# Kernel optimization log

Measured on AMD Instinct MI355X. Metric: run time of the kernel, lower is better.

Reference implementation:

```python
import jax, jax.numpy as jnp
import numpy as np

N = 12288
IN_C = 64
OUT_C = 64
NEG_INF = -1.0e9

def setup_inputs() -> dict:
    key = jax.random.key(0)
    k1, k2, k3, k4 = jax.random.split(key, 4)
    x = jax.random.normal(k1, (N, IN_C), dtype=jnp.float32)
    edge_index = jax.random.randint(k2, (N, N), 0, 2, dtype=jnp.int32)
    # xavier-ish scaling for params
    weight_w = jax.random.normal(k3, (IN_C, OUT_C), dtype=jnp.float32) * (1.0 / np.sqrt(IN_C))
    weight_a = jax.random.normal(k4, (2 * OUT_C, 1), dtype=jnp.float32) * (1.0 / np.sqrt(OUT_C))
    bias = jnp.zeros((OUT_C,), dtype=jnp.float32)
    return {"x": x, "edge_index": edge_index, "weight_w": weight_w,
            "weight_a": weight_a, "bias": bias}

def reference(x, edge_index, weight_w, weight_a, bias):
    wh = x @ weight_w                              # [N, out]
    a_src = weight_a[:OUT_C, 0]                    # [out]
    a_dst = weight_a[OUT_C:, 0]                    # [out]
    # rank-1 additive score: e[i,j] = <wh_i, a_src> + <wh_j, a_dst>
    e = (wh @ a_src)[:, None] + (wh @ a_dst)[None, :]   # [N, N]
    e = jax.nn.leaky_relu(e, negative_slope=0.01)        # torch LeakyReLU default
    scores = jnp.where(edge_index > 0, e, NEG_INF)
    attention = jax.nn.softmax(scores, axis=1)           # row-wise
    out = attention @ wh                                  # [N, out]
    return out + bias
```

## Files before the change

### kernel.cpp

```cpp
#include <hip/hip_runtime.h>
#include <hip/hip_bf16.h>
#include <cstddef>
#include <cstdint>

#define Nn 12288
#define MSTRIDE 264
#define DSTOFF (2 * 16 * MSTRIDE)
#define LOG2E 1.44269504088896340736f

typedef __bf16 bf16x8 __attribute__((ext_vector_type(8)));
typedef float  f32x4  __attribute__((ext_vector_type(4)));
typedef int    i32x4  __attribute__((ext_vector_type(4)));

__device__ __forceinline__ void gload_lds16_nt(const void* g, void* l) {
    __builtin_amdgcn_global_load_lds(
        (const __attribute__((address_space(1))) void*)g,
        (__attribute__((address_space(3))) void*)l, 16, 0, 2 );
}
__device__ __forceinline__ void gload_lds4(const void* g, void* l) {
    __builtin_amdgcn_global_load_lds(
        (const __attribute__((address_space(1))) void*)g,
        (__attribute__((address_space(3))) void*)l, 4, 0, 0);
}

__global__ __launch_bounds__(256) void prep_kernel(
    const float* __restrict__ x, const float* __restrict__ W,
    const float* __restrict__ wa, __bf16* __restrict__ whB,
    float* __restrict__ src, float* __restrict__ dst)
{
    __shared__ float  Wl[64 * 64];
    __shared__ float  Xl[64 * 64];
    __shared__ __bf16 whl[64 * 72];
    int t = threadIdx.x;
    int R0 = blockIdx.x * 64;
    for (int i = t; i < 4096; i += 256) {
        Wl[i] = W[i];
        Xl[i] = x[(size_t)R0 * 64 + i];
    }
    __syncthreads();
    int c   = t & 63;
    int r16 = (t >> 6) * 16;
    float vals[16];
    #pragma unroll
    for (int k = 0; k < 16; ++k) vals[k] = 0.f;
    #pragma unroll 16
    for (int kk = 0; kk < 64; ++kk) {
        float wv = Wl[kk * 64 + c];
        #pragma unroll
        for (int k = 0; k < 16; ++k)
            vals[k] = fmaf(Xl[(r16 + k) * 64 + kk], wv, vals[k]);
    }
    #pragma unroll
    for (int k = 0; k < 16; ++k) whl[c * 72 + r16 + k] = (__bf16)vals[k];
    __syncthreads();
    if (t < 64) {
        float s = 0.f, d = 0.f;
        #pragma unroll 16
        for (int cc = 0; cc < 64; ++cc) {
            float v = (float)whl[cc * 72 + t];
            s = fmaf(v, wa[cc], s);
            d = fmaf(v, wa[64 + cc], d);
        }
        src[R0 + t] = s * LOG2E;
        dst[R0 + t] = d * LOG2E;
    }
    #pragma unroll
    for (int gg = 0; gg < 2; ++gg) {
        int gidx   = t * 2 + gg;
        int jc_loc = gidx >> 8;
        int q      = (gidx >> 6) & 3;
        int lane   = gidx & 63;
        int crow   = (lane & 15) + 16 * q;
        int jrow   = jc_loc * 32 + (lane >> 4) * 8;
        bf16x8 v = *(const bf16x8*)&whl[crow * 72 + jrow];
        int jc = blockIdx.x * 2 + jc_loc;
        *(bf16x8*)&whB[((size_t)(jc * 4 + q) * 64 + lane) * 8] = v;
    }
}

__global__ __launch_bounds__(256) void attn_kernel(
    const int* __restrict__ mask, const __bf16* __restrict__ whB,
    const float* __restrict__ src, const float* __restrict__ dstv,
    const float* __restrict__ bias, float* __restrict__ out)
{
    __shared__ int lm[DSTOFF + 2 * 256];

    int t    = threadIdx.x;
    int lane = t & 63;
    int wid  = t >> 6;
    int g    = blockIdx.x;
    int row  = lane & 15;
    int kg   = lane >> 4;
    int jl   = kg * 8;

    float srow = src[g * 16 + row];
    asm volatile("" :: "v"(srow));

    bf16x8 vones;
    #pragma unroll
    for (int e = 0; e < 8; ++e) vones[e] = (__bf16)1.0f;

    i32x4 bset[2][8];
    f32x4 acc0 = {0.f, 0.f, 0.f, 0.f}, acc1 = acc0, acc2 = acc0, acc3 = acc0;
    f32x4 accZ = acc0;

#define STAGE(B, TT)                                                          \
    do {                                                                      \
        _Pragma("unroll")                                                     \
        for (int rr = 0; rr < 4; ++rr) {                                      \
            int rs = wid * 4 + rr;                                            \
            gload_lds16_nt(mask + (size_t)(g * 16 + rs) * Nn + (TT) * 256 +   \
                               lane * 4,                                      \
                           &lm[(B) * 4224 + rs * MSTRIDE]);                   \
        }                                                                     \
        gload_lds4(dstv + (TT) * 256 + wid * 64 + lane,                       \
                   &lm[DSTOFF + (B) * 256 + wid * 64]);                       \
    } while (0)

#define BLOAD(P, TT)                                                          \
    do {                                                                      \
        const char* _b0 = (const char*)whB +                                  \
                          ((size_t)((TT) * 8 + wid * 2)) * 4096 +             \
                          (size_t)lane * 16;                                  \
        const char* _b1 = _b0 + 4096;                                         \
        asm volatile("global_load_dwordx4 %0, %1, off"                        \
                     : "=v"(bset[P][0]) : "v"(_b0));                          \
        asm volatile("global_load_dwordx4 %0, %1, off offset:1024"            \
                     : "=v"(bset[P][1]) : "v"(_b0));                          \
        asm volatile("global_load_dwordx4 %0, %1, off offset:2048"            \
                     : "=v"(bset[P][2]) : "v"(_b0));                          \
        asm volatile("global_load_dwordx4 %0, %1, off offset:3072"            \
                     : "=v"(bset[P][3]) : "v"(_b0));                          \
        asm volatile("global_load_dwordx4 %0, %1, off"                        \
                     : "=v"(bset[P][4]) : "v"(_b1));                          \
        asm volatile("global_load_dwordx4 %0, %1, off offset:1024"            \
                     : "=v"(bset[P][5]) : "v"(_b1));                          \
        asm volatile("global_load_dwordx4 %0, %1, off offset:2048"            \
                     : "=v"(bset[P][6]) : "v"(_b1));                          \
        asm volatile("global_load_dwordx4 %0, %1, off offset:3072"            \
                     : "=v"(bset[P][7]) : "v"(_b1));                          \
    } while (0)

#define COMPUTE(TT, B, P)                                                     \
    do {                                                                      \
        const int*   mb = &lm[(B) * 4224 + row * MSTRIDE + wid * 64];         \
        const float* db = (const float*)&lm[DSTOFF + (B) * 256 + wid * 64];   \
        _Pragma("unroll")                                                     \
        for (int cc = 0; cc < 2; ++cc) {                                      \
            i32x4 m0 = *(const i32x4*)(mb + cc * 32 + jl);                    \
            i32x4 m1 = *(const i32x4*)(mb + cc * 32 + jl + 4);                \
            f32x4 d0 = *(const f32x4*)(db + cc * 32 + jl);                    \
            f32x4 d1 = *(const f32x4*)(db + cc * 32 + jl + 4);                \
            bf16x8 pa;                                                        \
            _Pragma("unroll")                                                 \
            for (int e = 0; e < 4; ++e) {                                     \
                float t0 = srow + d0[e];                                      \
                float f0 = fmaxf(t0, 0.01f * t0);                             \
                float w0 = __builtin_amdgcn_exp2f(f0);                        \
                w0 = (m0[e] > 0) ? w0 : 0.f;                                  \
                pa[e] = (__bf16)w0;                                           \
                float t1 = srow + d1[e];                                      \
                float f1 = fmaxf(t1, 0.01f * t1);                             \
                float w1 = __builtin_amdgcn_exp2f(f1);                        \
                w1 = (m1[e] > 0) ? w1 : 0.f;                                  \
                pa[4 + e] = (__bf16)w1;                                       \
            }                                                                 \
            acc0 = __builtin_amdgcn_mfma_f32_16x16x32_bf16(                   \
                pa, __builtin_bit_cast(bf16x8, bset[P][cc * 4 + 0]), acc0, 0, 0, 0); \
            acc1 = __builtin_amdgcn_mfma_f32_16x16x32_bf16(                   \
                pa, __builtin_bit_cast(bf16x8, bset[P][cc * 4 + 1]), acc1, 0, 0, 0); \
            acc2 = __builtin_amdgcn_mfma_f32_16x16x32_bf16(                   \
                pa, __builtin_bit_cast(bf16x8, bset[P][cc * 4 + 2]), acc2, 0, 0, 0); \
            acc3 = __builtin_amdgcn_mfma_f32_16x16x32_bf16(                   \
                pa, __builtin_bit_cast(bf16x8, bset[P][cc * 4 + 3]), acc3, 0, 0, 0); \
            accZ = __builtin_amdgcn_mfma_f32_16x16x32_bf16(                   \
                pa, vones, accZ, 0, 0, 0);                                    \
        }                                                                     \
    } while (0)

#define BODY_FULL(P)                                                          \
    do {                                                                      \
        STAGE((P) ^ 1, tt + 1);                                               \
        BLOAD((P) ^ 1, tt + 1);                                               \
        asm volatile("s_waitcnt vmcnt(13)" ::: "memory");                     \
        __builtin_amdgcn_sched_barrier(0);                                    \
        __builtin_amdgcn_s_barrier();                                         \
        __builtin_amdgcn_sched_barrier(0);                                    \
        COMPUTE(tt, P, P);                                                    \
        __builtin_amdgcn_s_barrier();                                         \
        ++tt;                                                                 \
    } while (0)

    int tt = 0;
    STAGE(0, 0);
    BLOAD(0, 0);

    for (int it = 0; it < 23; ++it) {
        BODY_FULL(0);
        BODY_FULL(1);
    }
    BODY_FULL(0);
    asm volatile("s_waitcnt vmcnt(0)" ::: "memory");
    __builtin_amdgcn_sched_barrier(0);
    __builtin_amdgcn_s_barrier();
    __builtin_amdgcn_sched_barrier(0);
    COMPUTE(47, 1, 1);

#undef BODY_FULL
#undef COMPUTE
#undef BLOAD
#undef STAGE

    __syncthreads();
    float* red  = (float*)lm;
    float* redz = red + 4096;
    #pragma unroll
    for (int r = 0; r < 4; ++r) {
        int orow = kg * 4 + r;
        red[wid * 1024 + orow * 64 + row]      = acc0[r];
        red[wid * 1024 + orow * 64 + row + 16] = acc1[r];
        red[wid * 1024 + orow * 64 + row + 32] = acc2[r];
        red[wid * 1024 + orow * 64 + row + 48] = acc3[r];
    }
    if (row == 0) {
        #pragma unroll
        for (int r = 0; r < 4; ++r) redz[wid * 16 + kg * 4 + r] = accZ[r];
    }
    __syncthreads();
    #pragma unroll
    for (int k = 0; k < 4; ++k) {
        int idx = k * 256 + t;
        int i   = idx >> 6;
        float sv = red[idx] + red[1024 + idx] + red[2048 + idx] + red[3072 + idx];
        float z  = redz[i] + redz[16 + i] + redz[32 + i] + redz[48 + i];
        z = (z != 0.f) ? z : 1.f;
        out[(size_t)g * 1024 + idx] = sv / z + bias[idx & 63];
    }
}

extern "C" void kernel_launch(void* const* d_in, const int* in_sizes, int n_in,
                              void* d_out, int out_size, void* d_ws, size_t ws_size,
                              hipStream_t stream) {
    const float* x    = (const float*)d_in[0];
    const int*   mask = (const int*)d_in[1];
    const float* W    = (const float*)d_in[2];
    const float* wa   = (const float*)d_in[3];
    const float* bias = (const float*)d_in[4];
    float* out = (float*)d_out;

    char* ws = (char*)d_ws;
    const size_t whB_bytes = (size_t)Nn * 64 * 2;
    const size_t vec_bytes = (size_t)Nn * 4;
    __bf16* whB = (__bf16*)ws;
    float*  src = (float*)(ws + whB_bytes);
    float*  dst = (float*)(ws + whB_bytes + vec_bytes);

    prep_kernel<<<Nn / 64, 256, 0, stream>>>(x, W, wa, whB, src, dst);
    attn_kernel<<<Nn / 16, 256, 0, stream>>>(mask, whB, src, dst, bias, out);
}
```

Measured before the change: 141.8 us.

## Widen attention column tile to 384 with XOR-swizzled LDS mask staging

Enlarges each pipeline step from 256 to 384 mask columns, cutting the iteration count from 48 to 32. Mask rows are staged into LDS with an XOR swizzle instead of a padded stride, and the loads and WH-fragment registers grow to match. The masking is folded into the exponent argument (a large negative value before exp2) rather than a select after exp2, and occupancy is hinted at 3 blocks per CU. This trades more LDS and VGPR use for fewer barriers and loop iterations.

```diff
diff --git a/kernel.cpp b/kernel.cpp
--- a/kernel.cpp
+++ b/kernel.cpp
@@ -4,8 +4,8 @@
 #include <cstdint>
 
 #define Nn 12288
-#define MSTRIDE 264
-#define DSTOFF (2 * 16 * MSTRIDE)
+#define NTIL 32
+#define TJ 384
 #define LOG2E 1.44269504088896340736f
 
 typedef __bf16 bf16x8 __attribute__((ext_vector_type(8)));
@@ -78,12 +78,12 @@
     }
 }
 
-__global__ __launch_bounds__(256) void attn_kernel(
+__global__ __launch_bounds__(256, 3) void attn_kernel(
     const int* __restrict__ mask, const __bf16* __restrict__ whB,
     const float* __restrict__ src, const float* __restrict__ dstv,
     const float* __restrict__ bias, float* __restrict__ out)
 {
-    __shared__ int lm[DSTOFF + 2 * 256];
+    __shared__ int lm[13312];
 
     int t    = threadIdx.x;
     int lane = t & 63;
@@ -91,7 +91,6 @@
     int g    = blockIdx.x;
     int row  = lane & 15;
     int kg   = lane >> 4;
-    int jl   = kg * 8;
 
     float srow = src[g * 16 + row];
     asm volatile("" :: "v"(srow));
@@ -100,29 +99,50 @@
     #pragma unroll
     for (int e = 0; e < 8; ++e) vones[e] = (__bf16)1.0f;
 
-    i32x4 bset[2][8];
+    int moff[6];
+    #pragma unroll
+    for (int i = 0; i < 6; ++i) {
+        int k    = wid * 6 + i;
+        int f    = k * 1024 + lane * 16;
+        int r    = f / 1536;
+        int cpos = (f - r * 1536) >> 4;
+        int cg   = cpos ^ (r & 7);
+        moff[i]  = r * (Nn * 4) + cg * 16;
+    }
+    const char* mbase = (const char*)mask + (size_t)g * 16 * (Nn * 4);
+
+    int s = row & 7;
+    int mi0[3], mi1[3];
+    #pragma unroll
+    for (int cc = 0; cc < 3; ++cc) {
+        int cb  = wid * 24 + cc * 8;
+        mi0[cc] = row * 384 + (cb + ((kg * 2) ^ s)) * 4;
+        mi1[cc] = row * 384 + (cb + ((kg * 2 + 1) ^ s)) * 4;
+    }
+
+    i32x4 bset[2][12];
     f32x4 acc0 = {0.f, 0.f, 0.f, 0.f}, acc1 = acc0, acc2 = acc0, acc3 = acc0;
     f32x4 accZ = acc0;
 
 #define STAGE(B, TT)                                                          \
     do {                                                                      \
         _Pragma("unroll")                                                     \
-        for (int rr = 0; rr < 4; ++rr) {                                      \
-            int rs = wid * 4 + rr;                                            \
-            gload_lds16_nt(mask + (size_t)(g * 16 + rs) * Nn + (TT) * 256 +   \
-                               lane * 4,                                      \
-                           &lm[(B) * 4224 + rs * MSTRIDE]);                   \
-        }                                                                     \
-        gload_lds4(dstv + (TT) * 256 + wid * 64 + lane,                       \
-                   &lm[DSTOFF + (B) * 256 + wid * 64]);                       \
+        for (int i = 0; i < 6; ++i)                                           \
+            gload_lds16_nt(mbase + (size_t)(TT) * 1536 + moff[i],             \
+                           (char*)lm + (B) * 24576 + (wid * 6 + i) * 1024);   \
+        _Pragma("unroll")                                                     \
+        for (int jj = 0; jj < 2; ++jj)                                        \
+            gload_lds4(dstv + (TT) * 384 + (wid * 2 + jj) * 64 + lane,        \
+                       (char*)lm + 49152 + (B) * 2048 + (wid * 2 + jj) * 256);\
     } while (0)
 
 #define BLOAD(P, TT)                                                          \
     do {                                                                      \
         const char* _b0 = (const char*)whB +                                  \
-                          ((size_t)((TT) * 8 + wid * 2)) * 4096 +             \
+                          ((size_t)(TT) * 12 + wid * 3) * 4096 +              \
                           (size_t)lane * 16;                                  \
         const char* _b1 = _b0 + 4096;                                         \
+        const char* _b2 = _b0 + 8192;                                         \
         asm volatile("global_load_dwordx4 %0, %1, off"                        \
                      : "=v"(bset[P][0]) : "v"(_b0));                          \
         asm volatile("global_load_dwordx4 %0, %1, off offset:1024"            \
@@ -139,31 +159,37 @@
                      : "=v"(bset[P][6]) : "v"(_b1));                          \
         asm volatile("global_load_dwordx4 %0, %1, off offset:3072"            \
                      : "=v"(bset[P][7]) : "v"(_b1));                          \
-    } while (0)
-
-#define COMPUTE(TT, B, P)                                                     \
-    do {                                                                      \
-        const int*   mb = &lm[(B) * 4224 + row * MSTRIDE + wid * 64];         \
-        const float* db = (const float*)&lm[DSTOFF + (B) * 256 + wid * 64];   \
+        asm volatile("global_load_dwordx4 %0, %1, off"                        \
+                     : "=v"(bset[P][8]) : "v"(_b2));                          \
+        asm volatile("global_load_dwordx4 %0, %1, off offset:1024"            \
+                     : "=v"(bset[P][9]) : "v"(_b2));                          \
+        asm volatile("global_load_dwordx4 %0, %1, off offset:2048"            \
+                     : "=v"(bset[P][10]) : "v"(_b2));                         \
+        asm volatile("global_load_dwordx4 %0, %1, off offset:3072"            \
+                     : "=v"(bset[P][11]) : "v"(_b2));                         \
+    } while (0)
+
+#define COMPUTE(B, P)                                                         \
+    do {                                                                      \
         _Pragma("unroll")                                                     \
-        for (int cc = 0; cc < 2; ++cc) {                                      \
-            i32x4 m0 = *(const i32x4*)(mb + cc * 32 + jl);                    \
-            i32x4 m1 = *(const i32x4*)(mb + cc * 32 + jl + 4);                \
-            f32x4 d0 = *(const f32x4*)(db + cc * 32 + jl);                    \
-            f32x4 d1 = *(const f32x4*)(db + cc * 32 + jl + 4);                \
+        for (int cc = 0; cc < 3; ++cc) {                                      \
+            i32x4 m0 = *(const i32x4*)&lm[(B) * 6144 + mi0[cc]];              \
+            i32x4 m1 = *(const i32x4*)&lm[(B) * 6144 + mi1[cc]];              \
+            const float* db = (const float*)&lm[12288 + (B) * 512 +           \
+                                                wid * 96 + cc * 32 + kg * 8]; \
+            f32x4 d0 = *(const f32x4*)(db);                                   \
+            f32x4 d1 = *(const f32x4*)(db + 4);                               \
             bf16x8 pa;                                                        \
             _Pragma("unroll")                                                 \
             for (int e = 0; e < 4; ++e) {                                     \
-                float t0 = srow + d0[e];                                      \
-                float f0 = fmaxf(t0, 0.01f * t0);                             \
-                float w0 = __builtin_amdgcn_exp2f(f0);                        \
-                w0 = (m0[e] > 0) ? w0 : 0.f;                                  \
-                pa[e] = (__bf16)w0;                                           \
-                float t1 = srow + d1[e];                                      \
-                float f1 = fmaxf(t1, 0.01f * t1);                             \
-                float w1 = __builtin_amdgcn_exp2f(f1);                        \
-                w1 = (m1[e] > 0) ? w1 : 0.f;                                  \
-                pa[4 + e] = (__bf16)w1;                                       \
+                float f0 = srow + d0[e];                                      \
+                f0 = fmaxf(f0, 0.01f * f0);                                   \
+                f0 = (m0[e] > 0) ? f0 : -1000.f;                              \
+                pa[e] = (__bf16)__builtin_amdgcn_exp2f(f0);                   \
+                float f1 = srow + d1[e];                                      \
+                f1 = fmaxf(f1, 0.01f * f1);                                   \
+                f1 = (m1[e] > 0) ? f1 : -1000.f;                              \
+                pa[4 + e] = (__bf16)__builtin_amdgcn_exp2f(f1);               \
             }                                                                 \
             acc0 = __builtin_amdgcn_mfma_f32_16x16x32_bf16(                   \
                 pa, __builtin_bit_cast(bf16x8, bset[P][cc * 4 + 0]), acc0, 0, 0, 0); \
@@ -182,11 +208,11 @@
     do {                                                                      \
         STAGE((P) ^ 1, tt + 1);                                               \
         BLOAD((P) ^ 1, tt + 1);                                               \
-        asm volatile("s_waitcnt vmcnt(13)" ::: "memory");                     \
+        asm volatile("s_waitcnt vmcnt(20)" ::: "memory");                     \
         __builtin_amdgcn_sched_barrier(0);                                    \
         __builtin_amdgcn_s_barrier();                                         \
         __builtin_amdgcn_sched_barrier(0);                                    \
-        COMPUTE(tt, P, P);                                                    \
+        COMPUTE(P, P);                                                        \
         __builtin_amdgcn_s_barrier();                                         \
         ++tt;                                                                 \
     } while (0)
@@ -195,7 +221,7 @@
     STAGE(0, 0);
     BLOAD(0, 0);
 
-    for (int it = 0; it < 23; ++it) {
+    for (int it = 0; it < 15; ++it) {
         BODY_FULL(0);
         BODY_FULL(1);
     }
@@ -204,7 +230,7 @@
     __builtin_amdgcn_sched_barrier(0);
     __builtin_amdgcn_s_barrier();
     __builtin_amdgcn_sched_barrier(0);
-    COMPUTE(47, 1, 1);
+    COMPUTE(1, 1);
 
 #undef BODY_FULL
 #undef COMPUTE
```

Result: slower. 186.3 us (+31.3%).
